# Optimization experiments

Measured on AMD Instinct MI355X. Metric: run time of the kernel, lower is better.

Reference implementation:

```python
import jax, jax.numpy as jnp
import numpy as np

SOBEL_X = jnp.array([[-1., 0., 1.], [-2., 0., 2.], [-1., 0., 1.]], dtype=jnp.float32).reshape(1, 1, 3, 3)
SOBEL_Y = jnp.array([[-1., -2., -1.], [0., 0., 0.], [1., 2., 1.]], dtype=jnp.float32).reshape(1, 1, 3, 3)
KERNEL_MASK = jnp.ones((1, 1, 3, 3), dtype=jnp.float32)


def _conv(x, k):
    # x: (N,1,H,W), k: (1,1,3,3), SAME padding (matches torch padding=1)
    return jax.lax.conv_general_dilated(
        x, k, window_strides=(1, 1), padding='SAME',
        dimension_numbers=('NCHW', 'OIHW', 'NCHW'))


def setup_inputs() -> dict:
    key = jax.random.key(0)
    k1, k2, k3 = jax.random.split(key, 3)
    shape = (2, 6, 512, 512, 8)  # (B, T, H, W, F)
    prediction = jax.random.normal(k1, shape, dtype=jnp.float32)
    target = jax.random.normal(k2, shape, dtype=jnp.float32)
    mask = jax.random.randint(k3, shape, 0, 2, dtype=jnp.int32)
    return {"prediction": prediction, "target": target, "mask": mask}


def reference(prediction, target, mask):
    B, T, H, W, F = prediction.shape
    # (B,T,H,W,F) -> (B*T*F, 1, H, W)
    def to_nchw(x):
        return x.transpose(0, 1, 4, 2, 3).reshape(B * T * F, 1, H, W)

    mask_r = to_nchw(mask.astype(jnp.float32))
    pred_r = to_nchw(prediction)
    tgt_r = to_nchw(target)

    valid = (_conv(mask_r, KERNEL_MASK) == 9.0).astype(prediction.dtype)

    gx_p = _conv(pred_r, SOBEL_X) * valid
    gy_p = _conv(pred_r, SOBEL_Y) * valid
    gx_t = _conv(tgt_r, SOBEL_X) * valid
    gy_t = _conv(tgt_r, SOBEL_Y) * valid

    # mode == 'l1'
    loss = jnp.abs(gx_p - gx_t) + jnp.abs(gy_p - gy_t)
    # (B*T*F,1,H,W) -> (B,T,H,W,F)
    return loss.reshape(B, T, F, H, W).transpose(0, 1, 3, 4, 2)
```

## Files before the change

kernel.cpp:

```cpp
#include <hip/hip_runtime.h>


constexpr int H = 512, W = 512, F = 8;
constexpr int IMAGES = 12;
constexpr int SH = 8;
constexpr int STRIPS = H / SH;
constexpr int NIT = SH + 2;

typedef float f32x4 __attribute__((ext_vector_type(4)));

__global__ __launch_bounds__(256, 4) void sobel_loss_kernel(
    const float* __restrict__ pred,
    const float* __restrict__ tgt,
    const int*   __restrict__ mask,
    float*       __restrict__ out)
{
    const int tid  = threadIdx.x;
    const int lane = tid & 63;
    const int wid  = tid >> 6;

    const int bid   = blockIdx.x;
    const int img   = bid >> 8;
    const int rest  = bid & 255;
    const int quad  = rest & 3;
    const int strip = rest >> 2;
    const int h0    = strip * SH;

    const int p = lane >> 1;
    const int q = lane & 1;
    const int w = (quad * 4 + wid) * 32 + p;

    const size_t ibase = (size_t)img * ((size_t)H * W * F);
    const int voff = w * F + q * 4;
    const bool eL = (p == 0);
    const bool eR = (p == 31);
    const bool edge = eL || eR;
    const int wn   = eL ? (w > 0 ? w - 1 : 0) : (w < W - 1 ? w + 1 : W - 1);
    const int eoff = wn * F + q * 4;
    const bool win = (w > 0) & (w < W - 1);

    float4 bp[2], bt[2]; int4 bm[2];
    float4 bep[2], bet[2]; int4 bem[2];
    float4 hx[3], hs[3]; unsigned hm[3];

    bep[0] = bep[1] = bet[0] = bet[1] = make_float4(0.f, 0.f, 0.f, 0.f);
    bem[0] = bem[1] = make_int4(0, 0, 0, 0);

#define SUB4(a, b) make_float4((a).x - (b).x, (a).y - (b).y, (a).z - (b).z, (a).w - (b).w)

#define PREFETCH(NB, HNX)                                                     \
    {                                                                         \
        const int hraw = (HNX);                                               \
        const int hc = hraw < 0 ? 0 : (hraw >= H ? H - 1 : hraw);             \
        const size_t ro = ibase + (size_t)hc * (W * F);                       \
        bp[NB] = *(const float4*)(pred + ro + voff);                          \
        bt[NB] = *(const float4*)(tgt  + ro + voff);                          \
        bm[NB] = *(const int4*)(mask + ro + voff);                            \
        if (edge) {                                                           \
            bep[NB] = *(const float4*)(pred + ro + eoff);                     \
            bet[NB] = *(const float4*)(tgt  + ro + eoff);                     \
            bem[NB] = *(const int4*)(mask + ro + eoff);                       \
        }                                                                     \
    }

    PREFETCH(0, h0 - 1)

#define STEP(I)                                                               \
    {                                                                         \
        constexpr int i  = (I);                                               \
        constexpr int cb = i & 1;                         \
        constexpr int s2 = i % 3;           \
        constexpr int s1 = (i + 2) % 3;                          \
        constexpr int s0 = (i + 1) % 3;                          \
        const int hin = h0 - 1 + i;                                           \
        if constexpr (i < NIT - 1) PREFETCH(cb ^ 1, hin + 1)                  \
        const float4 d  = SUB4(bp[cb], bt[cb]);                               \
        const float4 ed = SUB4(bep[cb], bet[cb]);                             \
        const unsigned m  = (unsigned)(bm[cb].x | (bm[cb].y << 1) |           \
                                       (bm[cb].z << 2) | (bm[cb].w << 3));    \
        const unsigned em = (unsigned)(bem[cb].x | (bem[cb].y << 1) |         \
                                       (bem[cb].z << 2) | (bem[cb].w << 3));  \
        float4 dl, dr;                                                        \
        dl.x = __shfl_up(d.x, 2);   dl.y = __shfl_up(d.y, 2);                 \
        dl.z = __shfl_up(d.z, 2);   dl.w = __shfl_up(d.w, 2);                 \
        dr.x = __shfl_down(d.x, 2); dr.y = __shfl_down(d.y, 2);               \
        dr.z = __shfl_down(d.z, 2); dr.w = __shfl_down(d.w, 2);               \
        unsigned ml = (unsigned)__shfl_up((int)m, 2);                         \
        unsigned mr = (unsigned)__shfl_down((int)m, 2);                       \
        if (eL) { dl = ed; ml = em; }                                         \
        if (eR) { dr = ed; mr = em; }                                         \
        hx[s2] = SUB4(dr, dl);                                                \
        hs[s2] = make_float4(dl.x + 2.f * d.x + dr.x,                         \
                             dl.y + 2.f * d.y + dr.y,                         \
                             dl.z + 2.f * d.z + dr.z,                         \
                             dl.w + 2.f * d.w + dr.w);                        \
        hm[s2] = ml & m & mr;                                                 \
        if constexpr (i >= 2) {                                               \
            const int r = hin - 1;                 \
            unsigned vm = hm[0] & hm[1] & hm[2];                              \
            if (!win || r == 0 || r == H - 1) vm = 0u;                        \
            f32x4 o;                                                          \
            { const float gx = hx[s0].x + 2.f * hx[s1].x + hx[s2].x;          \
              const float gy = hs[s2].x - hs[s0].x;                           \
              o.x = (vm & 1u) ? (fabsf(gx) + fabsf(gy)) : 0.f; }              \
            { const float gx = hx[s0].y + 2.f * hx[s1].y + hx[s2].y;          \
              const float gy = hs[s2].y - hs[s0].y;                           \
              o.y = (vm & 2u) ? (fabsf(gx) + fabsf(gy)) : 0.f; }              \
            { const float gx = hx[s0].z + 2.f * hx[s1].z + hx[s2].z;          \
              const float gy = hs[s2].z - hs[s0].z;                           \
              o.z = (vm & 4u) ? (fabsf(gx) + fabsf(gy)) : 0.f; }              \
            { const float gx = hx[s0].w + 2.f * hx[s1].w + hx[s2].w;          \
              const float gy = hs[s2].w - hs[s0].w;                           \
              o.w = (vm & 8u) ? (fabsf(gx) + fabsf(gy)) : 0.f; }              \
            __builtin_nontemporal_store(o,                                    \
                (f32x4*)(out + ibase + (size_t)r * (W * F) + voff));          \
        }                                                                     \
    }

    STEP(0) STEP(1) STEP(2) STEP(3) STEP(4)
    STEP(5) STEP(6) STEP(7) STEP(8) STEP(9)

#undef STEP
#undef PREFETCH
#undef SUB4
}

extern "C" void kernel_launch(void* const* d_in, const int* in_sizes, int n_in,
                              void* d_out, int out_size, void* d_ws, size_t ws_size,
                              hipStream_t stream) {
    const float* pred = (const float*)d_in[0];
    const float* tgt  = (const float*)d_in[1];
    const int*   mask = (const int*)d_in[2];
    float*       out  = (float*)d_out;

    const int blocks = IMAGES * 4 * STRIPS;
    sobel_loss_kernel<<<blocks, 256, 0, stream>>>(pred, tgt, mask, out);
}
```

Baseline: 314.9 us.

## Compute one output row per block with XCD-interleaved block mapping

Replaces the per-block 8-row strip with a rolling register window by a one-row-per-block scheme that loads the three neighboring rows directly. Block indices are remapped in an 8-way interleave so consecutive rows go to the same die partition, relying on L2 for vertical reuse. This raises parallelism and removes the serial prefetch pipeline, but issues about three times the row loads per output and depends on cache hits to avoid extra HBM traffic.

Result: no change. 317.9 us (+0.9%).

```diff
diff --git a/kernel.cpp b/kernel.cpp
--- a/kernel.cpp
+++ b/kernel.cpp
@@ -3,13 +3,11 @@
 
 constexpr int H = 512, W = 512, F = 8;
 constexpr int IMAGES = 12;
-constexpr int SH = 8;
-constexpr int STRIPS = H / SH;
-constexpr int NIT = SH + 2;
+constexpr int NB = IMAGES * H * 4;
 
 typedef float f32x4 __attribute__((ext_vector_type(4)));
 
-__global__ __launch_bounds__(256, 4) void sobel_loss_kernel(
+__global__ __launch_bounds__(256) void sobel_loss_kernel(
     const float* __restrict__ pred,
     const float* __restrict__ tgt,
     const int*   __restrict__ mask,
@@ -19,67 +17,77 @@
     const int lane = tid & 63;
     const int wid  = tid >> 6;
 
-    const int bid   = blockIdx.x;
-    const int img   = bid >> 8;
-    const int rest  = bid & 255;
-    const int quad  = rest & 3;
-    const int strip = rest >> 2;
-    const int h0    = strip * SH;
+    const int b0  = blockIdx.x;
+    const int bid = (b0 & 7) * (NB >> 3) + (b0 >> 3);
+
+    const int img  = bid >> 11;
+    const int rest = bid & 2047;
+    const int r    = rest >> 2;
+    const int quad = rest & 3;
 
     const int p = lane >> 1;
     const int q = lane & 1;
-    const int w = (quad * 4 + wid) * 32 + p;
+    const int w = quad * 128 + wid * 32 + p;
 
     const size_t ibase = (size_t)img * ((size_t)H * W * F);
     const int voff = w * F + q * 4;
+    float* const orow = out + ibase + (size_t)r * (W * F) + voff;
+
+    if (r == 0 || r == H - 1) {
+        f32x4 z = {0.f, 0.f, 0.f, 0.f};
+        __builtin_nontemporal_store(z, (f32x4*)orow);
+        return;
+    }
+
     const bool eL = (p == 0);
     const bool eR = (p == 31);
     const bool edge = eL || eR;
-    const int wn   = eL ? (w > 0 ? w - 1 : 0) : (w < W - 1 ? w + 1 : W - 1);
-    const int eoff = wn * F + q * 4;
-    const bool win = (w > 0) & (w < W - 1);
+    const int  wn  = eL ? (w > 0 ? w - 1 : 0) : (w < W - 1 ? w + 1 : W - 1);
+    const int  eoff = wn * F + q * 4;
+    const bool win  = (w > 0) & (w < W - 1);
 
-    float4 bp[2], bt[2]; int4 bm[2];
-    float4 bep[2], bet[2]; int4 bem[2];
-    float4 hx[3], hs[3]; unsigned hm[3];
+    const size_t ro0 = ibase + (size_t)(r - 1) * (W * F);
+    const size_t ro1 = ibase + (size_t)(r    ) * (W * F);
+    const size_t ro2 = ibase + (size_t)(r + 1) * (W * F);
 
-    bep[0] = bep[1] = bet[0] = bet[1] = make_float4(0.f, 0.f, 0.f, 0.f);
-    bem[0] = bem[1] = make_int4(0, 0, 0, 0);
+    const float4 P0 = *(const float4*)(pred + ro0 + voff);
+    const float4 P1 = *(const float4*)(pred + ro1 + voff);
+    const float4 P2 = *(const float4*)(pred + ro2 + voff);
+    const float4 T0 = *(const float4*)(tgt  + ro0 + voff);
+    const float4 T1 = *(const float4*)(tgt  + ro1 + voff);
+    const float4 T2 = *(const float4*)(tgt  + ro2 + voff);
+    const int4   M0 = *(const int4*)(mask + ro0 + voff);
+    const int4   M1 = *(const int4*)(mask + ro1 + voff);
+    const int4   M2 = *(const int4*)(mask + ro2 + voff);
+
+    float4 EP0, EP1, EP2, ET0, ET1, ET2;
+    int4   EM0, EM1, EM2;
+    EP0 = EP1 = EP2 = ET0 = ET1 = ET2 = make_float4(0.f, 0.f, 0.f, 0.f);
+    EM0 = EM1 = EM2 = make_int4(0, 0, 0, 0);
+    if (edge) {
+        EP0 = *(const float4*)(pred + ro0 + eoff);
+        EP1 = *(const float4*)(pred + ro1 + eoff);
+        EP2 = *(const float4*)(pred + ro2 + eoff);
+        ET0 = *(const float4*)(tgt  + ro0 + eoff);
+        ET1 = *(const float4*)(tgt  + ro1 + eoff);
+        ET2 = *(const float4*)(tgt  + ro2 + eoff);
+        EM0 = *(const int4*)(mask + ro0 + eoff);
+        EM1 = *(const int4*)(mask + ro1 + eoff);
+        EM2 = *(const int4*)(mask + ro2 + eoff);
+    }
 
 #define SUB4(a, b) make_float4((a).x - (b).x, (a).y - (b).y, (a).z - (b).z, (a).w - (b).w)
+#define PACK(M) ((unsigned)((M).x | ((M).y << 1) | ((M).z << 2) | ((M).w << 3)))
 
-#define PREFETCH(NB, HNX)                                                     \
+    float4 hx0, hx1, hx2, hs0, hs1, hs2;
+    unsigned hm0, hm1, hm2;
+
+#define ROWOP(P, T, M, EP, ET, EM, HX, HS, HM)                                \
     {                                                                         \
-        const int hraw = (HNX);                                               \
-        const int hc = hraw < 0 ? 0 : (hraw >= H ? H - 1 : hraw);             \
-        const size_t ro = ibase + (size_t)hc * (W * F);                       \
-        bp[NB] = *(const float4*)(pred + ro + voff);                          \
-        bt[NB] = *(const float4*)(tgt  + ro + voff);                          \
-        bm[NB] = *(const int4*)(mask + ro + voff);                            \
-        if (edge) {                                                           \
-            bep[NB] = *(const float4*)(pred + ro + eoff);                     \
-            bet[NB] = *(const float4*)(tgt  + ro + eoff);                     \
-            bem[NB] = *(const int4*)(mask + ro + eoff);                       \
-        }                                                                     \
-    }
-
-    PREFETCH(0, h0 - 1)
-
-#define STEP(I)                                                               \
-    {                                                                         \
-        constexpr int i  = (I);                                               \
-        constexpr int cb = i & 1;                         \
-        constexpr int s2 = i % 3;           \
-        constexpr int s1 = (i + 2) % 3;                          \
-        constexpr int s0 = (i + 1) % 3;                          \
-        const int hin = h0 - 1 + i;                                           \
-        if constexpr (i < NIT - 1) PREFETCH(cb ^ 1, hin + 1)                  \
-        const float4 d  = SUB4(bp[cb], bt[cb]);                               \
-        const float4 ed = SUB4(bep[cb], bet[cb]);                             \
-        const unsigned m  = (unsigned)(bm[cb].x | (bm[cb].y << 1) |           \
-                                       (bm[cb].z << 2) | (bm[cb].w << 3));    \
-        const unsigned em = (unsigned)(bem[cb].x | (bem[cb].y << 1) |         \
-                                       (bem[cb].z << 2) | (bem[cb].w << 3));  \
+        const float4 d  = SUB4(P, T);                                         \
+        const float4 ed = SUB4(EP, ET);                                       \
+        const unsigned m  = PACK(M);                                          \
+        const unsigned em = PACK(EM);                                         \
         float4 dl, dr;                                                        \
         dl.x = __shfl_up(d.x, 2);   dl.y = __shfl_up(d.y, 2);                 \
         dl.z = __shfl_up(d.z, 2);   dl.w = __shfl_up(d.w, 2);                 \
@@ -89,40 +97,49 @@
         unsigned mr = (unsigned)__shfl_down((int)m, 2);                       \
         if (eL) { dl = ed; ml = em; }                                         \
         if (eR) { dr = ed; mr = em; }                                         \
-        hx[s2] = SUB4(dr, dl);                                                \
-        hs[s2] = make_float4(dl.x + 2.f * d.x + dr.x,                         \
-                             dl.y + 2.f * d.y + dr.y,                         \
-                             dl.z + 2.f * d.z + dr.z,                         \
-                             dl.w + 2.f * d.w + dr.w);                        \
-        hm[s2] = ml & m & mr;                                                 \
-        if constexpr (i >= 2) {                                               \
-            const int r = hin - 1;                 \
-            unsigned vm = hm[0] & hm[1] & hm[2];                              \
-            if (!win || r == 0 || r == H - 1) vm = 0u;                        \
-            f32x4 o;                                                          \
-            { const float gx = hx[s0].x + 2.f * hx[s1].x + hx[s2].x;          \
-              const float gy = hs[s2].x - hs[s0].x;                           \
-              o.x = (vm & 1u) ? (fabsf(gx) + fabsf(gy)) : 0.f; }              \
-            { const float gx = hx[s0].y + 2.f * hx[s1].y + hx[s2].y;          \
-              const float gy = hs[s2].y - hs[s0].y;                           \
-              o.y = (vm & 2u) ? (fabsf(gx) + fabsf(gy)) : 0.f; }              \
-            { const float gx = hx[s0].z + 2.f * hx[s1].z + hx[s2].z;          \
-              const float gy = hs[s2].z - hs[s0].z;                           \
-              o.z = (vm & 4u) ? (fabsf(gx) + fabsf(gy)) : 0.f; }              \
-            { const float gx = hx[s0].w + 2.f * hx[s1].w + hx[s2].w;          \
-              const float gy = hs[s2].w - hs[s0].w;                           \
-              o.w = (vm & 8u) ? (fabsf(gx) + fabsf(gy)) : 0.f; }              \
-            __builtin_nontemporal_store(o,                                    \
-                (f32x4*)(out + ibase + (size_t)r * (W * F) + voff));          \
-        }                                                                     \
+        HX = SUB4(dr, dl);                                                    \
+        HS = make_float4(dl.x + 2.f * d.x + dr.x,                             \
+                         dl.y + 2.f * d.y + dr.y,                             \
+                         dl.z + 2.f * d.z + dr.z,                             \
+                         dl.w + 2.f * d.w + dr.w);                            \
+        HM = ml & m & mr;                                                     \
     }
 
-    STEP(0) STEP(1) STEP(2) STEP(3) STEP(4)
-    STEP(5) STEP(6) STEP(7) STEP(8) STEP(9)
+    ROWOP(P0, T0, M0, EP0, ET0, EM0, hx0, hs0, hm0)
+    ROWOP(P1, T1, M1, EP1, ET1, EM1, hx1, hs1, hm1)
+    ROWOP(P2, T2, M2, EP2, ET2, EM2, hx2, hs2, hm2)
 
-#undef STEP
-#undef PREFETCH
+#undef ROWOP
+
+    unsigned vm = hm0 & hm1 & hm2;
+    if (!win) vm = 0u;
+
+    f32x4 o;
+    {
+        const float gx = hx0.x + 2.f * hx1.x + hx2.x;
+        const float gy = hs2.x - hs0.x;
+        o.x = (vm & 1u) ? (fabsf(gx) + fabsf(gy)) : 0.f;
+    }
+    {
+        const float gx = hx0.y + 2.f * hx1.y + hx2.y;
+        const float gy = hs2.y - hs0.y;
+        o.y = (vm & 2u) ? (fabsf(gx) + fabsf(gy)) : 0.f;
+    }
+    {
+        const float gx = hx0.z + 2.f * hx1.z + hx2.z;
+        const float gy = hs2.z - hs0.z;
+        o.z = (vm & 4u) ? (fabsf(gx) + fabsf(gy)) : 0.f;
+    }
+    {
+        const float gx = hx0.w + 2.f * hx1.w + hx2.w;
+        const float gy = hs2.w - hs0.w;
+        o.w = (vm & 8u) ? (fabsf(gx) + fabsf(gy)) : 0.f;
+    }
+
+    __builtin_nontemporal_store(o, (f32x4*)orow);
+
 #undef SUB4
+#undef PACK
 }
 
 extern "C" void kernel_launch(void* const* d_in, const int* in_sizes, int n_in,
@@ -133,6 +150,5 @@
     const int*   mask = (const int*)d_in[2];
     float*       out  = (float*)d_out;
 
-    const int blocks = IMAGES * 4 * STRIPS;
-    sobel_loss_kernel<<<blocks, 256, 0, stream>>>(pred, tgt, mask, out);
+    sobel_loss_kernel<<<NB, 256, 0, stream>>>(pred, tgt, mask, out);
 }
```
